# Kernel optimization log

Hardware: AMD Instinct MI355X
Metric: run time of the kernel (lower is better)

## Reference

```python
import jax, jax.numpy as jnp
import numpy as np

B_SZ, L, H, P = 16, 1024, 256, 256
DT_MIN, DT_MAX = 1e-3, 1e-1


def setup_inputs() -> dict:
    key = jax.random.key(0)
    ks = jax.random.split(key, 6)
    u = jax.random.normal(ks[0], (B_SZ, L, H), dtype=jnp.float32)
    # Stable diagonal init (stands in for HiPPO-LegS diag: negative real part,
    # spread imaginary parts) so exp(Lambda*Delta) has |.|<1 over long scans.
    Lambda_re = -0.5 * jnp.ones((P,), jnp.float32)
    Lambda_im = jnp.pi * jnp.arange(P, dtype=jnp.float32)
    Bp = jax.random.normal(ks[1], (P, H, 2), jnp.float32) / jnp.sqrt(2.0 * H)  # (P,H,2) real/imag
    Cp = jax.random.normal(ks[2], (H, P, 2), jnp.float32) / jnp.sqrt(2.0 * P)  # (H,P,2) real/imag
    D = jax.random.normal(ks[3], (H,), jnp.float32)
    log_step = (jax.random.uniform(ks[4], (P, 1), jnp.float32)
                * (jnp.log(DT_MAX) - jnp.log(DT_MIN)) + jnp.log(DT_MIN))
    return {"u": u, "Lambda_re": Lambda_re, "Lambda_im": Lambda_im,
            "B": Bp, "C": Cp, "D": D, "log_step": log_step}


def _binop(ei, ej):
    # S5 associative scan element: (A, Bu); compose linear recurrences.
    ai, bi = ei
    aj, bj = ej
    return aj * ai, aj * bi + bj


def reference(u, Lambda_re, Lambda_im, B, C, D, log_step):
    # clip_eigs=False, step_rescale=1.0, conj_sym=True, discretization='zoh'
    Lambda = Lambda_re + 1j * Lambda_im                     # (P,) complex
    B_tilde = B[..., 0] + 1j * B[..., 1]                    # (P,H) complex
    C_tilde = C[..., 0] + 1j * C[..., 1]                    # (H,P) complex
    Delta = jnp.exp(log_step[:, 0])                         # (P,)
    # ZOH discretization
    Lambda_bar = jnp.exp(Lambda * Delta)                    # (P,)
    B_bar = ((Lambda_bar - 1.0) / Lambda)[:, None] * B_tilde  # (P,H)
    # Input projection: (B, L, P) complex
    Bu = jnp.einsum('ph,blh->blp', B_bar, u.astype(B_bar.dtype))
    Lam = jnp.broadcast_to(Lambda_bar, Bu.shape)            # (B, L, P)
    # Parallel associative scan over time axis
    _, xs = jax.lax.associative_scan(_binop, (Lam, Bu), axis=1)  # states (B,L,P)
    # Output projection; conj_sym -> 2 * real part
    ys = 2.0 * jnp.einsum('hp,blp->blh', C_tilde, xs).real  # (B,L,H)
    return ys + D * u                                       # feedthrough
```

## Files before the change

kernel.cpp:

```cpp
#include <hip/hip_runtime.h>
#include <hip/hip_bf16.h>
#include <math.h>

#define BB     16
#define LSEQ   1024
#define HH     256
#define PP     256
#define MROWS  (BB*LSEQ)
#define LC     32
#define NC     (LSEQ/LC)
#define NCHUNK (BB*NC)

#define OFF_W2T  262144u
#define OFF_PW   524288u
#define OFF_CEND 655360u
#define OFF_CARR 1703936u
#define OFF_XS   2752512u

typedef __attribute__((ext_vector_type(8))) short short8;
typedef __attribute__((ext_vector_type(4))) float floatx4;

__device__ __forceinline__ float bf2f(unsigned hs) {
    union { unsigned u; float f; } v; v.u = hs << 16; return v.f;
}
__device__ __forceinline__ unsigned short f2bs(float f) {
    __hip_bfloat16 h = __float2bfloat16(f);
    union { __hip_bfloat16 h; unsigned short s; } v; v.h = h; return v.s;
}
__device__ __forceinline__ unsigned packbf(float r, float i) {
    return (unsigned)f2bs(r) | ((unsigned)f2bs(i) << 16);
}
__device__ __forceinline__ void async16(const void* g, void* l) {
    __builtin_amdgcn_global_load_lds(
        (const __attribute__((address_space(1))) unsigned*)g,
        (__attribute__((address_space(3))) unsigned*)l, 16, 0, 0);
}
__device__ __forceinline__ float2 lam_pow(float lr, float li, float dtt) {
    float m = expf(lr * dtt);
    return make_float2(m * cosf(li * dtt), m * sinf(li * dtt));
}

#define XSTR 140
__global__ __launch_bounds__(512, 2) void k_g1scan(
        const float* __restrict__ u, const float* __restrict__ Lr,
        const float* __restrict__ Li, const float* __restrict__ ls,
        const float* __restrict__ Bm, char* __restrict__ ws) {
    __shared__ char smem[35840];
    char* Asb = smem;
    char* Bsb = smem + 16384;
    unsigned short* X = (unsigned short*)smem;
    unsigned* X32 = (unsigned*)smem;
    const int tid = threadIdx.x, bx = blockIdx.x;
    const int ns = bx & 3, rg = bx >> 2;
    const int m0 = rg * 128, n0 = ns * 128;
    const int wave = tid >> 6, lane = tid & 63;
    const int q = lane >> 4, rr = lane & 15;

    const int pl = tid >> 3, oct = tid & 7;
    const int gpb = (n0 >> 1) + pl;
    float crc, cic;
    {
        float lr = Lr[gpb], li = Li[gpb];
        float dt = expf(ls[gpb]);
        float2 lam = lam_pow(lr, li, dt);
        float den = lr * lr + li * li;
        float nr = lam.x - 1.0f, ni = lam.y;
        crc = (nr * lr + ni * li) / den;
        cic = (ni * lr - nr * li) / den;
    }
    const int arow = tid >> 2, koff = (tid & 3) * 16;

    floatx4 acc[8];
    #pragma unroll
    for (int i = 0; i < 8; ++i) acc[i] = (floatx4)0.0f;

    for (int k0 = 0; k0 < 256; k0 += 64) {
        __syncthreads();
        {
            const float4* up = (const float4*)(u + (size_t)(m0 + arow) * 256 + k0 + koff);
            float4 v0 = up[0], v1 = up[1], v2 = up[2], v3 = up[3];
            char* dst = Asb + (koff >> 5) * 8192 + arow * 64 + (koff & 31) * 2;
            *(uint4*)dst = make_uint4(packbf(v0.x, v0.y), packbf(v0.z, v0.w),
                                      packbf(v1.x, v1.y), packbf(v1.z, v1.w));
            *(uint4*)(dst + 16) = make_uint4(packbf(v2.x, v2.y), packbf(v2.z, v2.w),
                                             packbf(v3.x, v3.y), packbf(v3.z, v3.w));
        }
        {
            const float4* bp = (const float4*)(Bm + ((size_t)gpb * 256 + k0 + oct * 8) * 2);
            float4 b0 = bp[0], b1 = bp[1], b2 = bp[2], b3 = bp[3];
            float re[8], im[8];
            re[0]=crc*b0.x-cic*b0.y; im[0]=crc*b0.y+cic*b0.x;
            re[1]=crc*b0.z-cic*b0.w; im[1]=crc*b0.w+cic*b0.z;
            re[2]=crc*b1.x-cic*b1.y; im[2]=crc*b1.y+cic*b1.x;
            re[3]=crc*b1.z-cic*b1.w; im[3]=crc*b1.w+cic*b1.z;
            re[4]=crc*b2.x-cic*b2.y; im[4]=crc*b2.y+cic*b2.x;
            re[5]=crc*b2.z-cic*b2.w; im[5]=crc*b2.w+cic*b2.z;
            re[6]=crc*b3.x-cic*b3.y; im[6]=crc*b3.y+cic*b3.x;
            re[7]=crc*b3.z-cic*b3.w; im[7]=crc*b3.w+cic*b3.z;
            int pan = oct >> 2, hh = (oct & 3) * 8;
            char* dr = Bsb + pan * 8192 + (2 * pl) * 64 + hh * 2;
            char* di = Bsb + pan * 8192 + (2 * pl + 1) * 64 + hh * 2;
            *(uint4*)dr = make_uint4(packbf(re[0], re[1]), packbf(re[2], re[3]),
                                     packbf(re[4], re[5]), packbf(re[6], re[7]));
            *(uint4*)di = make_uint4(packbf(im[0], im[1]), packbf(im[2], im[3]),
                                     packbf(im[4], im[5]), packbf(im[6], im[7]));
        }
        __syncthreads();
        #pragma unroll
        for (int ks = 0; ks < 2; ++ks) {
            short8 b = *(const short8*)(Bsb + ks * 8192 + (wave * 16 + rr) * 64 + q * 16);
            #pragma unroll
            for (int i = 0; i < 8; ++i) {
                short8 a = *(const short8*)(Asb + ks * 8192 + (i * 16 + rr) * 64 + q * 16);
                acc[i] = __builtin_amdgcn_mfma_f32_16x16x32_bf16(a, b, acc[i], 0, 0, 0);
            }
        }
    }
    __syncthreads();
    #pragma unroll
    for (int i = 0; i < 8; ++i)
        #pragma unroll
        for (int r0 = 0; r0 < 4; ++r0)
            X[(i * 16 + q * 4 + r0) * XSTR + wave * 16 + rr] = f2bs(acc[i][r0]);
    __syncthreads();

    if (tid < 256) {
        const int ch = tid >> 6, pq = tid & 63;
        const int gp = (n0 >> 1) + pq;
        const float2 lam = lam_pow(Lr[gp], Li[gp], expf(ls[gp]));
        unsigned* xs32 = (unsigned*)(ws + OFF_XS);
        float xr = 0.0f, xi = 0.0f;
        for (int j = 0; j < LC; ++j) {
            unsigned cv = X32[(ch * 32 + j) * (XSTR / 2) + pq];
            float br = bf2f(cv & 0xffffu), bi = bf2f(cv >> 16);
            float nr = fmaf(lam.x, xr, fmaf(-lam.y, xi, br));
            float ni = fmaf(lam.x, xi, fmaf(lam.y, xr, bi));
            xr = nr; xi = ni;
            xs32[(size_t)(m0 + ch * 32 + j) * 256 + gp] = packbf(xr, xi);
        }
        ((float2*)(ws + OFF_CEND))[(size_t)(rg * 4 + ch) * 256 + gp] = make_float2(xr, xi);
    }
}

__global__ void k_carry(const float* __restrict__ Lr, const float* __restrict__ Li,
                        const float* __restrict__ ls, const float* __restrict__ Cm,
                        char* __restrict__ ws) {
    const int tid = threadIdx.x, b = blockIdx.x;

    {
        int h = b * 16 + (tid >> 4);
        int p0 = (tid & 15) * 16;
        unsigned* w2 = (unsigned*)(ws + OFF_W2T);
        const float2* cp = (const float2*)Cm + (size_t)h * 256 + p0;
        #pragma unroll
        for (int e = 0; e < 16; ++e) {
            float2 c = cp[e];
            w2[(size_t)h * 256 + p0 + e] = packbf(2.0f * c.x, -2.0f * c.y);
        }
    }

    const int p = tid;
    const float lr = Lr[p], li = Li[p];
    const float dt = expf(ls[p]);

    {
        float2* pw = (float2*)(ws + OFF_PW);
        pw[(2 * b) * 256 + p]     = lam_pow(lr, li, dt * (float)(2 * b));
        pw[(2 * b + 1) * 256 + p] = lam_pow(lr, li, dt * (float)(2 * b + 1));
        if (b == 0) pw[32 * 256 + p] = lam_pow(lr, li, dt * 32.0f);
    }

    float2 g = lam_pow(lr, li, dt * (float)LC);
    const float2* cend = (const float2*)(ws + OFF_CEND);
    float2* carr = (float2*)(ws + OFF_CARR);
    float sr = 0.0f, si = 0.0f;
    for (int c = 0; c < NC; ++c) {
        size_t off = (size_t)(b * NC + c) * 256 + p;
        carr[off] = make_float2(sr, si);
        float2 e = cend[off];
        float nr = fmaf(g.x, sr, fmaf(-g.y, si, e.x));
        float ni = fmaf(g.x, si, fmaf(g.y, sr, e.y));
        sr = nr; si = ni;
    }
}

__global__ __launch_bounds__(256, 4) void k_gemm2fix(
        const char* __restrict__ ws_c, const float* __restrict__ D,
        const float* __restrict__ u, float* __restrict__ out) {
    __shared__ char Asb[8192];
    __shared__ char Bsb[16384];
    __shared__ float2 carrs[2][256];
    const unsigned short* W2 = (const unsigned short*)(ws_c + OFF_W2T);
    const unsigned* xs32 = (const unsigned*)(ws_c + OFF_XS);
    const float2* pw = (const float2*)(ws_c + OFF_PW);
    const float2* carr = (const float2*)(ws_c + OFF_CARR);

    const int tid = threadIdx.x;
    const int wave = tid >> 6, lane = tid & 63;
    const int q = lane >> 4, rr = lane & 15;
    const int c4 = lane & 3, r4 = lane >> 2;
    const int wm = wave & 1, wn = wave >> 1;
    const int m0 = blockIdx.y * 64, n0 = blockIdx.x * 128;

    {
        int cbase = m0 >> 5;
        carrs[0][tid] = carr[(size_t)cbase * 256 + tid];
        carrs[1][tid] = carr[(size_t)(cbase + 1) * 256 + tid];
    }

    floatx4 acc[2][4];
    #pragma unroll
    for (int i = 0; i < 2; ++i)
        #pragma unroll
        for (int j = 0; j < 4; ++j) acc[i][j] = (floatx4)0.0f;

    const int row = tid >> 2, qd = tid & 3;
    const int grow = m0 + row;
    const int jj = (grow & (LC - 1)) + 1;
    const int half = row >> 5;

    for (int k0 = 0; k0 < 512; k0 += 64) {
        __syncthreads();
        {
            int p0 = (k0 >> 1) + qd * 8;
            uint4 xa = *(const uint4*)(xs32 + (size_t)grow * 256 + p0);
            uint4 xb = *(const uint4*)(xs32 + (size_t)grow * 256 + p0 + 4);
            unsigned xv[8] = {xa.x, xa.y, xa.z, xa.w, xb.x, xb.y, xb.z, xb.w};
            const float2* pwp = pw + (size_t)jj * 256 + p0;
            const float2* cap = &carrs[half][p0];
            unsigned o[8];
            #pragma unroll
            for (int e = 0; e < 8; ++e) {
                float2 pwv = pwp[e];
                float2 cav = cap[e];
                float fr = pwv.x * cav.x - pwv.y * cav.y;
                float fi = pwv.x * cav.y + pwv.y * cav.x;
                o[e] = packbf(bf2f(xv[e] & 0xffffu) + fr, bf2f(xv[e] >> 16) + fi);
            }
            char* dst = Asb + (qd >> 1) * 4096 + row * 64 + (qd & 1) * 32;
            *(uint4*)dst        = make_uint4(o[0], o[1], o[2], o[3]);
            *(uint4*)(dst + 16) = make_uint4(o[4], o[5], o[6], o[7]);
        }
        #pragma unroll
        for (int t = 0; t < 4; ++t) {
            int idx = t * 4 + wave;
            int pan = idx & 1, rowg = idx >> 1;
            int rw = rowg * 16 + r4;
            async16(W2 + (size_t)(n0 + rw) * 512 + k0 + pan * 32 + c4 * 8,
                    Bsb + pan * 8192 + rw * 64 + c4 * 16);
        }
        __syncthreads();
        #pragma unroll
        for (int ks = 0; ks < 2; ++ks) {
            short8 a[2], bfr[4];
            #pragma unroll
            for (int i = 0; i < 2; ++i)
                a[i] = *(const short8*)(Asb + ks * 4096 +
                                        (wm * 32 + i * 16 + rr) * 64 + q * 16);
            #pragma unroll
            for (int j = 0; j < 4; ++j)
                bfr[j] = *(const short8*)(Bsb + ks * 8192 +
                                          ((wn * 64 + j * 16 + rr)) * 64 + q * 16);
            #pragma unroll
            for (int i = 0; i < 2; ++i)
                #pragma unroll
                for (int j = 0; j < 4; ++j)
                    acc[i][j] = __builtin_amdgcn_mfma_f32_16x16x32_bf16(a[i], bfr[j], acc[i][j], 0, 0, 0);
        }
    }

    #pragma unroll
    for (int i = 0; i < 2; ++i) {
        int mbase = m0 + wm * 32 + i * 16 + q * 4;
        #pragma unroll
        for (int j = 0; j < 4; ++j) {
            int col = n0 + wn * 64 + j * 16 + rr;
            #pragma unroll
            for (int r0 = 0; r0 < 4; ++r0) {
                int rw = mbase + r0;
                size_t gi = (size_t)rw * 256 + col;
                out[gi] = acc[i][j][r0] + D[col] * u[gi];
            }
        }
    }
}

extern "C" void kernel_launch(void* const* d_in, const int* in_sizes, int n_in,
                              void* d_out, int out_size, void* d_ws, size_t ws_size,
                              hipStream_t stream) {
    const float* u  = (const float*)d_in[0];
    const float* Lr = (const float*)d_in[1];
    const float* Li = (const float*)d_in[2];
    const float* Bm = (const float*)d_in[3];
    const float* Cm = (const float*)d_in[4];
    const float* D  = (const float*)d_in[5];
    const float* ls = (const float*)d_in[6];
    float* out = (float*)d_out;
    char* ws = (char*)d_ws;

    k_g1scan<<<512, 512, 0, stream>>>(u, Lr, Li, ls, Bm, ws);
    k_carry<<<BB, 256, 0, stream>>>(Lr, Li, ls, Cm, ws);
    k_gemm2fix<<<dim3(2, MROWS / 64), 256, 0, stream>>>(ws, D, u, out);
}
```

Before: 121.8 us.

## Remove carry kernel by recomputing chunk carries inside output GEMM

Drops the separate serial carry-propagation kernel. Each output GEMM block now recomputes its chunk carry directly from the chunk-end states, as a power-weighted sum over preceding chunks. The C-weight packing and lambda-power table move into the first kernel, which now uses wider 128x256 tiles with a 2x4 wave grid and half as many blocks. This saves a launch and a 16-block serial kernel, at the cost of redundant carry work in the GEMM blocks (up to 31 steps each) and higher LDS and register use in the first kernel.

```diff
diff --git a/kernel.cpp b/kernel.cpp
--- a/kernel.cpp
+++ b/kernel.cpp
@@ -14,7 +14,6 @@
 #define OFF_W2T  262144u
 #define OFF_PW   524288u
 #define OFF_CEND 655360u
-#define OFF_CARR 1703936u
 #define OFF_XS   2752512u
 
 typedef __attribute__((ext_vector_type(8))) short short8;
@@ -40,24 +39,36 @@
     return make_float2(m * cosf(li * dtt), m * sinf(li * dtt));
 }
 
-#define XSTR 140
-__global__ __launch_bounds__(512, 2) void k_g1scan(
+#define XSTR 264
+__global__ __launch_bounds__(512, 4) void k_g1scan(
         const float* __restrict__ u, const float* __restrict__ Lr,
         const float* __restrict__ Li, const float* __restrict__ ls,
-        const float* __restrict__ Bm, char* __restrict__ ws) {
-    __shared__ char smem[35840];
+        const float* __restrict__ Bm, const float* __restrict__ Cm,
+        char* __restrict__ ws) {
+    __shared__ char smem[49152];
     char* Asb = smem;
     char* Bsb = smem + 16384;
     unsigned short* X = (unsigned short*)smem;
     unsigned* X32 = (unsigned*)smem;
     const int tid = threadIdx.x, bx = blockIdx.x;
-    const int ns = bx & 3, rg = bx >> 2;
-    const int m0 = rg * 128, n0 = ns * 128;
+    const int nh = bx & 1, rg = bx >> 1;
+    const int m0 = rg * 128, n0 = nh * 256;
     const int wave = tid >> 6, lane = tid & 63;
     const int q = lane >> 4, rr = lane & 15;
-
-    const int pl = tid >> 3, oct = tid & 7;
-    const int gpb = (n0 >> 1) + pl;
+    const int wm = wave & 1, wn = wave >> 1;
+
+    if (tid < 256) {
+        float2 c = ((const float2*)Cm)[(size_t)bx * 256 + tid];
+        ((unsigned*)(ws + OFF_W2T))[(size_t)bx * 256 + tid] = packbf(2.0f * c.x, -2.0f * c.y);
+        if (bx < 33) {
+            float lr = Lr[tid], li = Li[tid];
+            ((float2*)(ws + OFF_PW))[bx * 256 + tid] =
+                lam_pow(lr, li, expf(ls[tid]) * (float)bx);
+        }
+    }
+
+    const int pl = tid >> 2, hq = tid & 3;
+    const int gpb = nh * 128 + pl;
     float crc, cic;
     {
         float lr = Lr[gpb], li = Li[gpb];
@@ -70,9 +81,11 @@
     }
     const int arow = tid >> 2, koff = (tid & 3) * 16;
 
-    floatx4 acc[8];
+    floatx4 acc[4][4];
     #pragma unroll
-    for (int i = 0; i < 8; ++i) acc[i] = (floatx4)0.0f;
+    for (int i = 0; i < 4; ++i)
+        #pragma unroll
+        for (int j = 0; j < 4; ++j) acc[i][j] = (floatx4)0.0f;
 
     for (int k0 = 0; k0 < 256; k0 += 64) {
         __syncthreads();
@@ -86,114 +99,97 @@
                                              packbf(v3.x, v3.y), packbf(v3.z, v3.w));
         }
         {
-            const float4* bp = (const float4*)(Bm + ((size_t)gpb * 256 + k0 + oct * 8) * 2);
-            float4 b0 = bp[0], b1 = bp[1], b2 = bp[2], b3 = bp[3];
-            float re[8], im[8];
-            re[0]=crc*b0.x-cic*b0.y; im[0]=crc*b0.y+cic*b0.x;
-            re[1]=crc*b0.z-cic*b0.w; im[1]=crc*b0.w+cic*b0.z;
-            re[2]=crc*b1.x-cic*b1.y; im[2]=crc*b1.y+cic*b1.x;
-            re[3]=crc*b1.z-cic*b1.w; im[3]=crc*b1.w+cic*b1.z;
-            re[4]=crc*b2.x-cic*b2.y; im[4]=crc*b2.y+cic*b2.x;
-            re[5]=crc*b2.z-cic*b2.w; im[5]=crc*b2.w+cic*b2.z;
-            re[6]=crc*b3.x-cic*b3.y; im[6]=crc*b3.y+cic*b3.x;
-            re[7]=crc*b3.z-cic*b3.w; im[7]=crc*b3.w+cic*b3.z;
-            int pan = oct >> 2, hh = (oct & 3) * 8;
-            char* dr = Bsb + pan * 8192 + (2 * pl) * 64 + hh * 2;
-            char* di = Bsb + pan * 8192 + (2 * pl + 1) * 64 + hh * 2;
-            *(uint4*)dr = make_uint4(packbf(re[0], re[1]), packbf(re[2], re[3]),
-                                     packbf(re[4], re[5]), packbf(re[6], re[7]));
-            *(uint4*)di = make_uint4(packbf(im[0], im[1]), packbf(im[2], im[3]),
-                                     packbf(im[4], im[5]), packbf(im[6], im[7]));
+            const float4* bp = (const float4*)(Bm + ((size_t)gpb * 256 + k0 + hq * 16) * 2);
+            int pan = hq >> 1, hh = (hq & 1) * 16;
+            char* dr = Bsb + pan * 16384 + (2 * pl) * 64 + hh * 2;
+            char* di = Bsb + pan * 16384 + (2 * pl + 1) * 64 + hh * 2;
+            #pragma unroll
+            for (int g2 = 0; g2 < 2; ++g2) {
+                float4 b0 = bp[g2 * 4 + 0], b1 = bp[g2 * 4 + 1];
+                float4 b2 = bp[g2 * 4 + 2], b3 = bp[g2 * 4 + 3];
+                float re[8], im[8];
+                re[0]=crc*b0.x-cic*b0.y; im[0]=crc*b0.y+cic*b0.x;
+                re[1]=crc*b0.z-cic*b0.w; im[1]=crc*b0.w+cic*b0.z;
+                re[2]=crc*b1.x-cic*b1.y; im[2]=crc*b1.y+cic*b1.x;
+                re[3]=crc*b1.z-cic*b1.w; im[3]=crc*b1.w+cic*b1.z;
+                re[4]=crc*b2.x-cic*b2.y; im[4]=crc*b2.y+cic*b2.x;
+                re[5]=crc*b2.z-cic*b2.w; im[5]=crc*b2.w+cic*b2.z;
+                re[6]=crc*b3.x-cic*b3.y; im[6]=crc*b3.y+cic*b3.x;
+                re[7]=crc*b3.z-cic*b3.w; im[7]=crc*b3.w+cic*b3.z;
+                *(uint4*)(dr + g2 * 16) = make_uint4(packbf(re[0], re[1]), packbf(re[2], re[3]),
+                                                     packbf(re[4], re[5]), packbf(re[6], re[7]));
+                *(uint4*)(di + g2 * 16) = make_uint4(packbf(im[0], im[1]), packbf(im[2], im[3]),
+                                                     packbf(im[4], im[5]), packbf(im[6], im[7]));
+            }
         }
         __syncthreads();
         #pragma unroll
         for (int ks = 0; ks < 2; ++ks) {
-            short8 b = *(const short8*)(Bsb + ks * 8192 + (wave * 16 + rr) * 64 + q * 16);
-            #pragma unroll
-            for (int i = 0; i < 8; ++i) {
-                short8 a = *(const short8*)(Asb + ks * 8192 + (i * 16 + rr) * 64 + q * 16);
-                acc[i] = __builtin_amdgcn_mfma_f32_16x16x32_bf16(a, b, acc[i], 0, 0, 0);
+            short8 a[4], b[4];
+            #pragma unroll
+            for (int i = 0; i < 4; ++i)
+                a[i] = *(const short8*)(Asb + ks * 8192 +
+                                        (wm * 64 + i * 16 + rr) * 64 + q * 16);
+            #pragma unroll
+            for (int j = 0; j < 4; ++j)
+                b[j] = *(const short8*)(Bsb + ks * 16384 +
+                                        (wn * 64 + j * 16 + rr) * 64 + q * 16);
+            #pragma unroll
+            for (int i = 0; i < 4; ++i)
+                #pragma unroll
+                for (int j = 0; j < 4; ++j)
+                    acc[i][j] = __builtin_amdgcn_mfma_f32_16x16x32_bf16(a[i], b[j], acc[i][j], 0, 0, 0);
+        }
+    }
+
+    unsigned* xs32 = (unsigned*)(ws + OFF_XS);
+    const int pq = tid & 127, ch = (tid >> 7) & 1;
+    const int gp = nh * 128 + pq;
+    float2 lam;
+    if (tid < 256) lam = lam_pow(Lr[gp], Li[gp], expf(ls[gp]));
+    #pragma unroll
+    for (int s = 0; s < 2; ++s) {
+        __syncthreads();
+        if (wm == s) {
+            #pragma unroll
+            for (int i = 0; i < 4; ++i)
+                #pragma unroll
+                for (int j = 0; j < 4; ++j)
+                    #pragma unroll
+                    for (int r0 = 0; r0 < 4; ++r0)
+                        X[(i * 16 + q * 4 + r0) * XSTR + wn * 64 + j * 16 + rr] =
+                            f2bs(acc[i][j][r0]);
+        }
+        __syncthreads();
+        if (tid < 256) {
+            const int mrow = m0 + s * 64 + ch * 32;
+            float xr = 0.0f, xi = 0.0f;
+            for (int j = 0; j < LC; ++j) {
+                unsigned cv = X32[(ch * 32 + j) * (XSTR / 2) + pq];
+                float br = bf2f(cv & 0xffffu), bi = bf2f(cv >> 16);
+                float nr = fmaf(lam.x, xr, fmaf(-lam.y, xi, br));
+                float ni = fmaf(lam.x, xi, fmaf(lam.y, xr, bi));
+                xr = nr; xi = ni;
+                xs32[(size_t)(mrow + j) * 256 + gp] = packbf(xr, xi);
             }
-        }
-    }
-    __syncthreads();
-    #pragma unroll
-    for (int i = 0; i < 8; ++i)
-        #pragma unroll
-        for (int r0 = 0; r0 < 4; ++r0)
-            X[(i * 16 + q * 4 + r0) * XSTR + wave * 16 + rr] = f2bs(acc[i][r0]);
-    __syncthreads();
-
-    if (tid < 256) {
-        const int ch = tid >> 6, pq = tid & 63;
-        const int gp = (n0 >> 1) + pq;
-        const float2 lam = lam_pow(Lr[gp], Li[gp], expf(ls[gp]));
-        unsigned* xs32 = (unsigned*)(ws + OFF_XS);
-        float xr = 0.0f, xi = 0.0f;
-        for (int j = 0; j < LC; ++j) {
-            unsigned cv = X32[(ch * 32 + j) * (XSTR / 2) + pq];
-            float br = bf2f(cv & 0xffffu), bi = bf2f(cv >> 16);
-            float nr = fmaf(lam.x, xr, fmaf(-lam.y, xi, br));
-            float ni = fmaf(lam.x, xi, fmaf(lam.y, xr, bi));
-            xr = nr; xi = ni;
-            xs32[(size_t)(m0 + ch * 32 + j) * 256 + gp] = packbf(xr, xi);
-        }
-        ((float2*)(ws + OFF_CEND))[(size_t)(rg * 4 + ch) * 256 + gp] = make_float2(xr, xi);
-    }
-}
-
-__global__ void k_carry(const float* __restrict__ Lr, const float* __restrict__ Li,
-                        const float* __restrict__ ls, const float* __restrict__ Cm,
-                        char* __restrict__ ws) {
-    const int tid = threadIdx.x, b = blockIdx.x;
-
-    {
-        int h = b * 16 + (tid >> 4);
-        int p0 = (tid & 15) * 16;
-        unsigned* w2 = (unsigned*)(ws + OFF_W2T);
-        const float2* cp = (const float2*)Cm + (size_t)h * 256 + p0;
-        #pragma unroll
-        for (int e = 0; e < 16; ++e) {
-            float2 c = cp[e];
-            w2[(size_t)h * 256 + p0 + e] = packbf(2.0f * c.x, -2.0f * c.y);
-        }
-    }
-
-    const int p = tid;
-    const float lr = Lr[p], li = Li[p];
-    const float dt = expf(ls[p]);
-
-    {
-        float2* pw = (float2*)(ws + OFF_PW);
-        pw[(2 * b) * 256 + p]     = lam_pow(lr, li, dt * (float)(2 * b));
-        pw[(2 * b + 1) * 256 + p] = lam_pow(lr, li, dt * (float)(2 * b + 1));
-        if (b == 0) pw[32 * 256 + p] = lam_pow(lr, li, dt * 32.0f);
-    }
-
-    float2 g = lam_pow(lr, li, dt * (float)LC);
-    const float2* cend = (const float2*)(ws + OFF_CEND);
-    float2* carr = (float2*)(ws + OFF_CARR);
-    float sr = 0.0f, si = 0.0f;
-    for (int c = 0; c < NC; ++c) {
-        size_t off = (size_t)(b * NC + c) * 256 + p;
-        carr[off] = make_float2(sr, si);
-        float2 e = cend[off];
-        float nr = fmaf(g.x, sr, fmaf(-g.y, si, e.x));
-        float ni = fmaf(g.x, si, fmaf(g.y, sr, e.y));
-        sr = nr; si = ni;
+            ((float2*)(ws + OFF_CEND))[(size_t)(rg * 4 + s * 2 + ch) * 256 + gp] =
+                make_float2(xr, xi);
+        }
     }
 }
 
 __global__ __launch_bounds__(256, 4) void k_gemm2fix(
         const char* __restrict__ ws_c, const float* __restrict__ D,
-        const float* __restrict__ u, float* __restrict__ out) {
+        const float* __restrict__ u, float* __restrict__ out,
+        const float* __restrict__ Lr, const float* __restrict__ Li,
+        const float* __restrict__ ls) {
     __shared__ char Asb[8192];
     __shared__ char Bsb[16384];
     __shared__ float2 carrs[2][256];
     const unsigned short* W2 = (const unsigned short*)(ws_c + OFF_W2T);
     const unsigned* xs32 = (const unsigned*)(ws_c + OFF_XS);
     const float2* pw = (const float2*)(ws_c + OFF_PW);
-    const float2* carr = (const float2*)(ws_c + OFF_CARR);
+    const float2* cend = (const float2*)(ws_c + OFF_CEND);
 
     const int tid = threadIdx.x;
     const int wave = tid >> 6, lane = tid & 63;
@@ -203,9 +199,23 @@
     const int m0 = blockIdx.y * 64, n0 = blockIdx.x * 128;
 
     {
-        int cbase = m0 >> 5;
-        carrs[0][tid] = carr[(size_t)cbase * 256 + tid];
-        carrs[1][tid] = carr[(size_t)(cbase + 1) * 256 + tid];
+        const int cbase = m0 >> 5;
+        const int b = cbase >> 5, c = cbase & 31;
+        const int p = tid;
+        const float2 g = lam_pow(Lr[p], Li[p], expf(ls[p]) * (float)LC);
+        float sr = 0.0f, si = 0.0f;
+        float gpr = 1.0f, gpi = 0.0f;
+        for (int k = 0; k < c; ++k) {
+            float2 e = cend[(size_t)(b * NC + (c - 1 - k)) * 256 + p];
+            sr = fmaf(gpr, e.x, fmaf(-gpi, e.y, sr));
+            si = fmaf(gpr, e.y, fmaf(gpi, e.x, si));
+            float t = gpr * g.x - gpi * g.y;
+            gpi = gpr * g.y + gpi * g.x; gpr = t;
+        }
+        carrs[0][p] = make_float2(sr, si);
+        float2 e = cend[(size_t)cbase * 256 + p];
+        carrs[1][p] = make_float2(fmaf(g.x, sr, fmaf(-g.y, si, e.x)),
+                                  fmaf(g.x, si, fmaf(g.y, sr, e.y)));
     }
 
     floatx4 acc[2][4];
@@ -298,7 +308,6 @@
     float* out = (float*)d_out;
     char* ws = (char*)d_ws;
 
-    k_g1scan<<<512, 512, 0, stream>>>(u, Lr, Li, ls, Bm, ws);
-    k_carry<<<BB, 256, 0, stream>>>(Lr, Li, ls, Cm, ws);
-    k_gemm2fix<<<dim3(2, MROWS / 64), 256, 0, stream>>>(ws, D, u, out);
-}
+    k_g1scan<<<256, 512, 0, stream>>>(u, Lr, Li, ls, Bm, Cm, ws);
+    k_gemm2fix<<<dim3(2, MROWS / 64), 256, 0, stream>>>(ws, D, u, out, Lr, Li, ls);
+}
```

New measurement: 119.1 us. 1.02x faster.
